# Kernel tuning notes

Hardware: AMD Instinct MI355X
Metric: run time of the kernel (lower is better)

The kernel has to match this reference:

```python
import jax, jax.numpy as jnp
import numpy as np

B, L1, L2 = 4, 1024, 512
D_PG, D_EX = 2304, 1024
H, HKV, DH = 8, 4, 256
SCALE = 256.0 ** -0.5


def _rope(x, cos, sin):
    # x: [B, L, h, DH]; cos/sin: [B, L, 1, DH//2]
    x = x.astype(jnp.float32)
    x1, x2 = jnp.split(x, 2, axis=-1)
    return jnp.concatenate([x1 * cos - x2 * sin, x2 * cos + x1 * sin], axis=-1)


def setup_inputs() -> dict:
    key = jax.random.key(0)
    ks = jax.random.split(key, 16)
    s = 0.02
    return {
        "pg_embeds": jax.random.normal(ks[0], (B, L1, D_PG), jnp.float32),
        "ex_embeds": jax.random.normal(ks[1], (B, L2, D_EX), jnp.float32),
        "cos": jax.random.normal(ks[2], (B, L1 + L2, 1, DH // 2), jnp.float32),
        "sin": jax.random.normal(ks[3], (B, L1 + L2, 1, DH // 2), jnp.float32),
        "attention_mask": jnp.zeros((B, L1 + L2, L1 + L2), jnp.float32),
        "Wq0": jax.random.normal(ks[4], (H * DH, D_PG), jnp.float32) * s,
        "Wk0": jax.random.normal(ks[5], (HKV * DH, D_PG), jnp.float32) * s,
        "Wv0": jax.random.normal(ks[6], (HKV * DH, D_PG), jnp.float32) * s,
        "Wo0": jax.random.normal(ks[7], (D_PG, H * DH), jnp.float32) * s,
        "Wq1": jax.random.normal(ks[8], (H * DH, D_EX), jnp.float32) * s,
        "Wk1": jax.random.normal(ks[9], (HKV * DH, D_EX), jnp.float32) * s,
        "Wv1": jax.random.normal(ks[10], (HKV * DH, D_EX), jnp.float32) * s,
        "Wo1": jax.random.normal(ks[11], (D_EX, H * DH), jnp.float32) * s,
    }


def reference(pg_embeds, ex_embeds, cos, sin, attention_mask,
              Wq0, Wk0, Wv0, Wo0, Wq1, Wk1, Wv1, Wo1):
    b, l1 = pg_embeds.shape[0], pg_embeds.shape[1]
    l2 = ex_embeds.shape[1]
    # per-stream QKV projections, then concat along sequence
    q = jnp.concatenate([
        (pg_embeds @ Wq0.T).reshape(b, l1, H, DH),
        (ex_embeds @ Wq1.T).reshape(b, l2, H, DH)], axis=1)
    k = jnp.concatenate([
        (pg_embeds @ Wk0.T).reshape(b, l1, HKV, DH),
        (ex_embeds @ Wk1.T).reshape(b, l2, HKV, DH)], axis=1)
    v = jnp.concatenate([
        (pg_embeds @ Wv0.T).reshape(b, l1, HKV, DH),
        (ex_embeds @ Wv1.T).reshape(b, l2, HKV, DH)], axis=1)
    q = _rope(q, cos, sin)  # fp32
    k = _rope(k, cos, sin)
    # GQA: repeat KV heads to match query heads
    rep = H // HKV
    k = jnp.repeat(k, rep, axis=2)
    v = jnp.repeat(jnp.repeat(v, rep, axis=2).astype(jnp.float32), 1, axis=0)
    # scores: [B, H, L, L]
    scores = jnp.einsum('bqhd,bkhd->bhqk', q, k) * SCALE
    scores = scores + attention_mask[:, None, :, :]
    p = jax.nn.softmax(scores, axis=-1)
    att = jnp.einsum('bhqk,bkhd->bqhd', p, v).reshape(b, l1 + l2, H * DH)
    out0 = att[:, :l1] @ Wo0.T
    out1 = att[:, l1:] @ Wo1.T
    return (out0, out1)
```

## Files before the change

kernel.cpp:

```cpp
#include <hip/hip_runtime.h>
#include <stdint.h>
#include <stddef.h>


typedef _Float16 f16;
typedef _Float16 f16x8 __attribute__((ext_vector_type(8)));
typedef _Float16 f16x4 __attribute__((ext_vector_type(4)));
typedef float    f32x4 __attribute__((ext_vector_type(4)));

__device__ __forceinline__ void async_ld16(const void* g, void* l) {
  __builtin_amdgcn_global_load_lds((const __attribute__((address_space(1))) void*)g,
                                   (__attribute__((address_space(3))) void*)l,
                                   16, 0, 0);
}

__device__ __forceinline__ int xswz(int bid, int n) {
  return (bid & 7) * (n >> 3) + (bid >> 3);
}

template <typename Epi>
__device__ __forceinline__ void gemm_pipe(f16* lds,
    const f16* __restrict__ A, int lda,
    const f16* __restrict__ B, int ldb,
    int K, Epi&& epi)
{
  const int t    = threadIdx.x;
  const int w    = t >> 6;
  const int lane = t & 63;
  const int q4   = lane >> 4;
  const int l16  = lane & 15;
  const int wm   = w >> 1;
  const int wn   = w & 1;

  const int srow = w * 16 + (lane >> 2);
  const int scol = (lane & 3) * 8;
  const f16* aP = A + (size_t)srow * lda + scol;
  const f16* bP = B + (size_t)srow * ldb + scol;
  const size_t a128 = (size_t)128 * lda;
  const int wl = w * 512;

  const int arow = (wm * 64 + l16) * 32 + q4 * 8;
  const int brow = (wn * 64 + l16) * 32 + q4 * 8;

  f32x4 acc[4][4];
  const f32x4 vz = {0.f, 0.f, 0.f, 0.f};
#pragma unroll
  for (int i = 0; i < 4; ++i)
#pragma unroll
    for (int j = 0; j < 4; ++j) acc[i][j] = vz;

#define STAGE3(kt, bi)                                            \
  { const int kk_ = (kt) << 5; f16* d_ = lds + (bi) * 12288;      \
    async_ld16(aP + kk_,        d_ + wl);                         \
    async_ld16(aP + a128 + kk_, d_ + 4096 + wl);                  \
    async_ld16(bP + kk_,        d_ + 8192 + wl); }

  STAGE3(0, 0);
  asm volatile("" ::: "memory");
  STAGE3(1, 1);

  const int NT = K >> 5;
  int cur = 0;
  for (int tk = 0; tk < NT; ++tk) {
    if (tk == NT - 1) asm volatile("s_waitcnt vmcnt(0)" ::: "memory");
    else              asm volatile("s_waitcnt vmcnt(3)" ::: "memory");
    asm volatile("s_barrier" ::: "memory");

    const f16* aS = lds + cur * 12288;
    const f16* bS = aS + 8192;
    f16x8 af[4], bf[4];
#pragma unroll
    for (int i = 0; i < 4; ++i) {
      af[i] = *(const f16x8*)(aS + arow + i * 512);
      bf[i] = *(const f16x8*)(bS + brow + i * 512);
    }
    if (tk + 2 < NT) {
      int nb = cur + 2; if (nb >= 3) nb -= 3;
      STAGE3(tk + 2, nb);
    }
    __builtin_amdgcn_s_setprio(1);
#pragma unroll
    for (int mi = 0; mi < 4; ++mi)
#pragma unroll
      for (int ni = 0; ni < 4; ++ni)
        acc[mi][ni] = __builtin_amdgcn_mfma_f32_16x16x32_f16(af[mi], bf[ni], acc[mi][ni], 0, 0, 0);
    __builtin_amdgcn_s_setprio(0);
    asm volatile("s_barrier" ::: "memory");
    ++cur; if (cur == 3) cur = 0;
  }
#undef STAGE3

#pragma unroll
  for (int mi = 0; mi < 4; ++mi)
#pragma unroll
    for (int ni = 0; ni < 4; ++ni)
#pragma unroll
      for (int r = 0; r < 4; ++r)
        epi(wm * 64 + mi * 16 + q4 * 4 + r, wn * 64 + ni * 16 + l16, acc[mi][ni][r]);
}

__global__ __launch_bounds__(512, 4) void k_qkv4(
    const f16* __restrict__ xpg, const f16* __restrict__ xex,
    const f16* __restrict__ W0,  const f16* __restrict__ W1,
    f16* __restrict__ q, f16* __restrict__ k, f16* __restrict__ v)
{
  __shared__ alignas(16) f16 lds[36864];
  const int idx = xswz(blockIdx.x, 768);
  int by, bx, K; const f16 *A, *B;
  const bool s0 = idx < 512;
  if (s0) { by = idx >> 5; bx = idx & 31; K = 2304;
            A = xpg + (size_t)by * 256 * 2304; B = W0 + (size_t)bx * 128 * 2304; }
  else    { int j = idx - 512; by = j >> 5; bx = j & 31; K = 1024;
            A = xex + (size_t)by * 256 * 1024; B = W1 + (size_t)bx * 128 * 1024; }

  f16* D; int ldd, coff;
  if (bx < 16)      { D = q; ldd = 2048; coff = 0; }
  else if (bx < 24) { D = k; ldd = 1024; coff = 2048; }
  else              { D = v; ldd = 1024; coff = 3072; }
  const int colb = bx * 128 - coff;
  const int rowb = s0 ? ((by >> 2) * 1536 + (by & 3) * 256)
                      : ((by >> 1) * 1536 + 1024 + (by & 1) * 256);

  gemm_pipe(lds, A, K, B, K, K, [&](int r, int c, float fv) {
    D[(size_t)(rowb + r) * ldd + colb + c] = (f16)fv;
  });
}

__global__ __launch_bounds__(256) void k_post(
    f16* __restrict__ q, f16* __restrict__ k,
    const float* __restrict__ cs, const float* __restrict__ sn,
    const float* __restrict__ msk, f16* __restrict__ mkh,
    const f16* __restrict__ v, f16* __restrict__ vt)
{
  const int blk = blockIdx.x;
  if (blk < 6144) {
    __shared__ f16 tile[32][33];
    const int b = blk / 1536, r0 = blk % 1536;
    const int d0 = (r0 & 31) * 32, l0 = (r0 >> 5) * 32;
    const int t = threadIdx.x;
    const int tr = t >> 5, tc = t & 31;
#pragma unroll
    for (int i = 0; i < 4; ++i)
      tile[tr + i * 8][tc] = v[((size_t)b * 1536 + l0 + tr + i * 8) * 1024 + d0 + tc];
    __syncthreads();
#pragma unroll
    for (int i = 0; i < 4; ++i) {
      int d = d0 + tr + i * 8;
      vt[(((size_t)b * 4 + (d >> 8)) * 256 + (d & 255)) * 1536 + l0 + tc] = tile[tc][tr + i * 8];
    }
  } else if (blk < 15360) {
    const size_t gid = ((size_t)(blk - 6144) * 256 + threadIdx.x) * 4;
    float4 m4 = *(const float4*)(msk + gid);
    f16x4 o = {(f16)m4.x, (f16)m4.y, (f16)m4.z, (f16)m4.w};
    *(f16x4*)(mkh + gid) = o;
  } else {
    const size_t tid8 = ((size_t)(blk - 15360) * 256 + threadIdx.x) * 8;
    f16* base; size_t row; int col;
    if (tid8 < 12582912ull) { base = q + tid8; row = tid8 >> 11; col = (int)(tid8 & 2047); }
    else { size_t f = tid8 - 12582912ull; base = k + f; row = f >> 10; col = (int)(f & 1023); }
    const int j0 = (col & 255) >> 1;
    f16x8 x = *(const f16x8*)base;
    float4 c4 = *(const float4*)(cs + row * 128 + j0);
    float4 s4 = *(const float4*)(sn + row * 128 + j0);
    f16x8 o;
    const float cc[4] = {c4.x, c4.y, c4.z, c4.w};
    const float ss[4] = {s4.x, s4.y, s4.z, s4.w};
#pragma unroll
    for (int p = 0; p < 4; ++p) {
      float x1 = (float)x[2 * p], x2 = (float)x[2 * p + 1];
      o[2 * p]     = (f16)(x1 * cc[p] - x2 * ss[p]);
      o[2 * p + 1] = (f16)(x2 * cc[p] + x1 * ss[p]);
    }
    *(f16x8*)base = o;
  }
}

__global__ __launch_bounds__(512, 4) void k_attn3(
    const f16* __restrict__ qb, const f16* __restrict__ kb,
    const f16* __restrict__ mask, f16* __restrict__ Sdst,
    const f16* __restrict__ Psrc, const f16* __restrict__ vt,
    f16* __restrict__ att0, f16* __restrict__ att1,
    const f16* __restrict__ wo0, const f16* __restrict__ wo1,
    float* __restrict__ out0, float* __restrict__ out1,
    int b_sc, int b_pv, int b_op, int npv, int nop)
{
  __shared__ alignas(16) f16 lds[36864];
  const int idx = xswz(blockIdx.x, (int)gridDim.x);
  if (idx < nop) {
    int by, bx, ldc, rowb; const f16 *A, *B; float* C;
    if (idx < 72) { by = idx / 18; bx = idx % 18;
                    A = att0 + (size_t)(b_op * 4 + by) * 256 * 2048;
                    B = wo0 + (size_t)bx * 128 * 2048;
                    C = out0; ldc = 2304; rowb = b_op * 1024 + by * 256; }
    else          { int j = idx - 72; by = j >> 3; bx = j & 7;
                    A = att1 + (size_t)(b_op * 2 + by) * 256 * 2048;
                    B = wo1 + (size_t)bx * 128 * 2048;
                    C = out1; ldc = 1024; rowb = b_op * 512 + by * 256; }
    const int colb = bx * 128;
    gemm_pipe(lds, A, 2048, B, 2048, 2048, [&](int r, int c, float fv) {
      C[(size_t)(rowb + r) * ldc + colb + c] = fv;
    });
  } else if (idx < nop + npv) {
    const int j = idx - nop;
    const int h = j / 12, rem = j % 12, by = rem >> 1, bx = rem & 1;
    const f16* A = Psrc + (size_t)h * 1536 * 1536 + (size_t)by * 256 * 1536;
    const f16* B = vt + (size_t)(b_pv * 4 + (h >> 1)) * 256 * 1536 + (size_t)bx * 128 * 1536;
    f16* dst = (by < 4)
      ? att0 + (size_t)(b_pv * 1024 + by * 256) * 2048 + h * 256 + bx * 128
      : att1 + (size_t)(b_pv * 512 + (by - 4) * 256) * 2048 + h * 256 + bx * 128;
    gemm_pipe(lds, A, 1536, B, 1536, 1536, [&](int r, int c, float fv) {
      dst[(size_t)r * 2048 + c] = (f16)fv;
    });
  } else {
    const int j = idx - nop - npv;
    const int h = j / 72, rem = j % 72, by = rem / 12, bx = rem % 12;
    const f16* A = qb + (size_t)b_sc * 1536 * 2048 + h * 256 + (size_t)by * 256 * 2048;
    const f16* B = kb + (size_t)b_sc * 1536 * 1024 + (h >> 1) * 256 + (size_t)bx * 128 * 1024;
    f16* Sz = Sdst + (size_t)h * 1536 * 1536 + (size_t)by * 256 * 1536 + bx * 128;
    const f16* mb = mask + (size_t)b_sc * 1536 * 1536 + (size_t)by * 256 * 1536 + bx * 128;
    gemm_pipe(lds, A, 2048, B, 1024, 256, [&](int r, int c, float fv) {
      size_t i = (size_t)r * 1536 + c;
      Sz[i] = (f16)(fv * 0.0625f + (float)mb[i]);
    });
  }
}

__global__ __launch_bounds__(256) void k_softmax(f16* __restrict__ S)
{
  const int row = blockIdx.x * 4 + (threadIdx.x >> 6);
  const int lane = threadIdx.x & 63;
  f16* p = S + (size_t)row * 1536 + lane * 8;
  f16x8 v0 = *(const f16x8*)p;
  f16x8 v1 = *(const f16x8*)(p + 512);
  f16x8 v2 = *(const f16x8*)(p + 1024);
  float x[24];
#pragma unroll
  for (int i = 0; i < 8; ++i) {
    x[i] = (float)v0[i]; x[8 + i] = (float)v1[i]; x[16 + i] = (float)v2[i];
  }
  float mx = x[0];
#pragma unroll
  for (int i = 1; i < 24; ++i) mx = fmaxf(mx, x[i]);
#pragma unroll
  for (int o = 32; o > 0; o >>= 1) mx = fmaxf(mx, __shfl_xor(mx, o, 64));
  float s = 0.f;
#pragma unroll
  for (int i = 0; i < 24; ++i) { x[i] = __expf(x[i] - mx); s += x[i]; }
#pragma unroll
  for (int o = 32; o > 0; o >>= 1) s += __shfl_xor(s, o, 64);
  const float inv = 1.f / s;
  f16x8 o0, o1, o2;
#pragma unroll
  for (int i = 0; i < 8; ++i) {
    o0[i] = (f16)(x[i] * inv); o1[i] = (f16)(x[8 + i] * inv); o2[i] = (f16)(x[16 + i] * inv);
  }
  *(f16x8*)p = o0; *(f16x8*)(p + 512) = o1; *(f16x8*)(p + 1024) = o2;
}

__global__ __launch_bounds__(256) void k_cast_all(
    const float* __restrict__ s0, const float* __restrict__ s1,
    const float* __restrict__ s2, const float* __restrict__ s3,
    const float* __restrict__ s4, const float* __restrict__ s5,
    f16* __restrict__ ws)
{
  const size_t gid = ((size_t)blockIdx.x * 256 + threadIdx.x) * 4;
  const float* s; size_t off, dst;
  if      (gid < 9437184ull)  { s = s0; off = gid;               dst = 0ull        + off; }
  else if (gid < 11534336ull) { s = s1; off = gid - 9437184ull;  dst = 9437184ull  + off; }
  else if (gid < 13893632ull) { s = s2; off = gid - 11534336ull; dst = 18612224ull + off; }
  else if (gid < 18612224ull) { s = s3; off = gid - 13893632ull; dst = 20971520ull + off; }
  else if (gid < 19660800ull) { s = s4; off = gid - 18612224ull; dst = 28835840ull + off; }
  else                        { s = s5; off = gid - 19660800ull; dst = 29884416ull + off; }
  float4 v = *(const float4*)(s + off);
  f16x4 o = {(f16)v.x, (f16)v.y, (f16)v.z, (f16)v.w};
  *(f16x4*)(ws + dst) = o;
}

__global__ __launch_bounds__(256) void k_cast_wr(
    const float* __restrict__ wq0, const float* __restrict__ wk0,
    const float* __restrict__ wq1, const float* __restrict__ wk1,
    f16* __restrict__ W0c, f16* __restrict__ W1c)
{
  const int idx = blockIdx.x;
  const float* src; f16* dstm; int K, r, drow;
  if      (idx < 2048) { src = wq0; dstm = W0c; K = 2304; r = idx;        drow = idx; }
  else if (idx < 3072) { src = wk0; dstm = W0c; K = 2304; r = idx - 2048; drow = idx; }
  else if (idx < 5120) { src = wq1; dstm = W1c; K = 1024; r = idx - 3072; drow = idx - 3072; }
  else                 { src = wk1; dstm = W1c; K = 1024; r = idx - 5120; drow = idx - 3072; }
  const int w = r & 255;
  const int srow = (r & ~255) + (w >> 1) + ((w & 1) << 7);
  const float* sp = src + (size_t)srow * K;
  f16* dp = dstm + (size_t)drow * K;
  for (int c = threadIdx.x * 4; c < K; c += 1024) {
    float4 v = *(const float4*)(sp + c);
    f16x4 o = {(f16)v.x, (f16)v.y, (f16)v.z, (f16)v.w};
    *(f16x4*)(dp + c) = o;
  }
}

extern "C" void kernel_launch(void* const* d_in, const int* in_sizes, int n_in,
                              void* d_out, int out_size, void* d_ws, size_t ws_size,
                              hipStream_t stream)
{
  (void)in_sizes; (void)n_in; (void)out_size; (void)ws_size;
  const float* pg  = (const float*)d_in[0];
  const float* ex  = (const float*)d_in[1];
  const float* cs  = (const float*)d_in[2];
  const float* sn  = (const float*)d_in[3];
  const float* msk = (const float*)d_in[4];

  char* ws = (char*)d_ws;
  f16* xpg  = (f16*)(ws + 0);
  f16* xex  = (f16*)(ws + 18874368);
  f16* W0c  = (f16*)(ws + 23068672);
  f16* wo0c = (f16*)(ws + 41943040);
  f16* W1c  = (f16*)(ws + 51380224);
  f16* wo1c = (f16*)(ws + 59768832);
  f16* qb   = (f16*)(ws + 63963136);
  f16* kb   = (f16*)(ws + 89128960);
  f16* vb   = (f16*)(ws + 101711872);
  f16* vt   = (f16*)(ws + 114294784);
  f16* att0 = (f16*)(ws + 126877696);
  f16* att1 = (f16*)(ws + 143654912);
  f16* S0   = (f16*)(ws + 152043520);
  f16* S1   = (f16*)(ws + 189792256);
  f16* mkh  = W0c;
  float* out0 = (float*)d_out;
  float* out1 = out0 + 9437184;

  k_cast_all<<<21248, 256, 0, stream>>>(
      pg, ex, (const float*)d_in[7], (const float*)d_in[8],
      (const float*)d_in[11], (const float*)d_in[12], (f16*)ws);
  k_cast_wr<<<6144, 256, 0, stream>>>(
      (const float*)d_in[5], (const float*)d_in[6],
      (const float*)d_in[9], (const float*)d_in[10], W0c, W1c);

  k_qkv4<<<768, 512, 0, stream>>>(xpg, xex, W0c, W1c, qb, kb, vb);

  k_post<<<24576, 256, 0, stream>>>(qb, kb, cs, sn, msk, mkh, vb, vt);

  k_attn3<<<576, 512, 0, stream>>>(qb, kb, mkh, S0, S0, vt, att0, att1, wo0c, wo1c, out0, out1, 0, 0, 0, 0, 0);
  k_softmax<<<3072, 256, 0, stream>>>(S0);
  k_attn3<<<672, 512, 0, stream>>>(qb, kb, mkh, S1, S0, vt, att0, att1, wo0c, wo1c, out0, out1, 1, 0, 0, 96, 0);
  k_softmax<<<3072, 256, 0, stream>>>(S1);
  k_attn3<<<760, 512, 0, stream>>>(qb, kb, mkh, S0, S1, vt, att0, att1, wo0c, wo1c, out0, out1, 2, 1, 0, 96, 88);
  k_softmax<<<3072, 256, 0, stream>>>(S0);
  k_attn3<<<760, 512, 0, stream>>>(qb, kb, mkh, S1, S0, vt, att0, att1, wo0c, wo1c, out0, out1, 3, 2, 1, 96, 88);
  k_softmax<<<3072, 256, 0, stream>>>(S1);

  k_attn3<<<184, 512, 0, stream>>>(qb, kb, mkh, S0, S1, vt, att0, att1, wo0c, wo1c, out0, out1, 0, 3, 2, 96, 88);
  k_attn3<<<88, 512, 0, stream>>>(qb, kb, mkh, S0, S1, vt, att0, att1, wo0c, wo1c, out0, out1, 0, 0, 3, 0, 88);
}
```

Measured before the change: 757.1 us.

## Enlarge GEMM tiles to 256x256 with double-buffered 64-wide K steps

Replaces the 256x128 triple-buffered GEMM core with a 256x256 tile that stages 64 K-elements per iteration into a double buffer, with each wave computing 128x64. Grid sizes for the QKV, QK^T, PV and output projection phases are halved, and the XCD block swizzle is dropped. The goal is more reuse per byte loaded into LDS and fewer blocks. In exchange it uses 128 KB LDS per block and twice the accumulators, which lowers occupancy to two blocks per CU. Small grids such as 44 or 92 blocks may also underfill the 256 CUs.

```diff
diff --git a/kernel.cpp b/kernel.cpp
--- a/kernel.cpp
+++ b/kernel.cpp
@@ -14,12 +14,8 @@
                                    16, 0, 0);
 }
 
-__device__ __forceinline__ int xswz(int bid, int n) {
-  return (bid & 7) * (n >> 3) + (bid >> 3);
-}
-
 template <typename Epi>
-__device__ __forceinline__ void gemm_pipe(f16* lds,
+__device__ __forceinline__ void gemm256(f16* lds,
     const f16* __restrict__ A, int lda,
     const f16* __restrict__ B, int ldb,
     int K, Epi&& epi)
@@ -29,99 +25,107 @@
   const int lane = t & 63;
   const int q4   = lane >> 4;
   const int l16  = lane & 15;
-  const int wm   = w >> 1;
-  const int wn   = w & 1;
-
-  const int srow = w * 16 + (lane >> 2);
-  const int scol = (lane & 3) * 8;
-  const f16* aP = A + (size_t)srow * lda + scol;
-  const f16* bP = B + (size_t)srow * ldb + scol;
-  const size_t a128 = (size_t)128 * lda;
-  const int wl = w * 512;
-
-  const int arow = (wm * 64 + l16) * 32 + q4 * 8;
+  const int wm   = w >> 2;
+  const int wn   = w & 3;
+
+  f16* ldsA = lds;
+  f16* ldsB = lds + 32768;
+
+  const f16* aP = A + (size_t)(lane >> 2) * lda + (lane & 3) * 8;
+  const f16* bP = B + (size_t)(lane >> 2) * ldb + (lane & 3) * 8;
+  const size_t aR0 = (size_t)(w * 32) * lda;
+  const size_t aR1 = aR0 + (size_t)16 * lda;
+  const size_t bR0 = (size_t)(w * 32) * ldb;
+  const size_t bR1 = bR0 + (size_t)16 * ldb;
+  const int wo = w * 1024;
+
+  const int arow = (wm * 128 + l16) * 32 + q4 * 8;
   const int brow = (wn * 64 + l16) * 32 + q4 * 8;
 
-  f32x4 acc[4][4];
+  f32x4 acc[8][4];
   const f32x4 vz = {0.f, 0.f, 0.f, 0.f};
 #pragma unroll
-  for (int i = 0; i < 4; ++i)
+  for (int i = 0; i < 8; ++i)
 #pragma unroll
     for (int j = 0; j < 4; ++j) acc[i][j] = vz;
 
-#define STAGE3(kt, bi)                                            \
-  { const int kk_ = (kt) << 5; f16* d_ = lds + (bi) * 12288;      \
-    async_ld16(aP + kk_,        d_ + wl);                         \
-    async_ld16(aP + a128 + kk_, d_ + 4096 + wl);                  \
-    async_ld16(bP + kk_,        d_ + 8192 + wl); }
-
-  STAGE3(0, 0);
-  asm volatile("" ::: "memory");
-  STAGE3(1, 1);
-
-  const int NT = K >> 5;
-  int cur = 0;
+#pragma unroll
+  for (int s = 0; s < 2; ++s) {
+    const int kk = s * 32;
+    async_ld16(aP + aR0 + kk, ldsA + s * 8192 + wo);
+    async_ld16(aP + aR1 + kk, ldsA + s * 8192 + wo + 512);
+    async_ld16(bP + bR0 + kk, ldsB + s * 8192 + wo);
+    async_ld16(bP + bR1 + kk, ldsB + s * 8192 + wo + 512);
+  }
+
+  const int NT = K >> 6;
   for (int tk = 0; tk < NT; ++tk) {
-    if (tk == NT - 1) asm volatile("s_waitcnt vmcnt(0)" ::: "memory");
-    else              asm volatile("s_waitcnt vmcnt(3)" ::: "memory");
-    asm volatile("s_barrier" ::: "memory");
-
-    const f16* aS = lds + cur * 12288;
-    const f16* bS = aS + 8192;
-    f16x8 af[4], bf[4];
-#pragma unroll
-    for (int i = 0; i < 4; ++i) {
-      af[i] = *(const f16x8*)(aS + arow + i * 512);
-      bf[i] = *(const f16x8*)(bS + brow + i * 512);
+    const int d  = (tk & 1) ? 16384 : 0;
+    const int dn = 16384 - d;
+    const bool st = tk + 1 < NT;
+    const int kn = (tk + 1) << 6;
+#pragma unroll
+    for (int s = 0; s < 2; ++s) {
+      if (s == 0 || st) asm volatile("s_waitcnt vmcnt(4)" ::: "memory");
+      else              asm volatile("s_waitcnt vmcnt(0)" ::: "memory");
+      asm volatile("s_barrier" ::: "memory");
+      const f16* aS = ldsA + d + s * 8192;
+      const f16* bS = ldsB + d + s * 8192;
+      f16x8 af[8], bf[4];
+#pragma unroll
+      for (int i = 0; i < 8; ++i) af[i] = *(const f16x8*)(aS + arow + i * 512);
+#pragma unroll
+      for (int i = 0; i < 4; ++i) bf[i] = *(const f16x8*)(bS + brow + i * 512);
+      if (st) {
+        const int kk = kn + s * 32;
+        async_ld16(aP + aR0 + kk, ldsA + dn + s * 8192 + wo);
+        async_ld16(aP + aR1 + kk, ldsA + dn + s * 8192 + wo + 512);
+        async_ld16(bP + bR0 + kk, ldsB + dn + s * 8192 + wo);
+        async_ld16(bP + bR1 + kk, ldsB + dn + s * 8192 + wo + 512);
+      }
+      __builtin_amdgcn_s_setprio(1);
+#pragma unroll
+      for (int mi = 0; mi < 8; ++mi)
+#pragma unroll
+        for (int ni = 0; ni < 4; ++ni)
+          acc[mi][ni] = __builtin_amdgcn_mfma_f32_16x16x32_f16(af[mi], bf[ni], acc[mi][ni], 0, 0, 0);
+      __builtin_amdgcn_s_setprio(0);
+      asm volatile("s_barrier" ::: "memory");
     }
-    if (tk + 2 < NT) {
-      int nb = cur + 2; if (nb >= 3) nb -= 3;
-      STAGE3(tk + 2, nb);
-    }
-    __builtin_amdgcn_s_setprio(1);
-#pragma unroll
-    for (int mi = 0; mi < 4; ++mi)
-#pragma unroll
-      for (int ni = 0; ni < 4; ++ni)
-        acc[mi][ni] = __builtin_amdgcn_mfma_f32_16x16x32_f16(af[mi], bf[ni], acc[mi][ni], 0, 0, 0);
-    __builtin_amdgcn_s_setprio(0);
-    asm volatile("s_barrier" ::: "memory");
-    ++cur; if (cur == 3) cur = 0;
-  }
-#undef STAGE3
-
-#pragma unroll
-  for (int mi = 0; mi < 4; ++mi)
+  }
+
+#pragma unroll
+  for (int mi = 0; mi < 8; ++mi)
 #pragma unroll
     for (int ni = 0; ni < 4; ++ni)
 #pragma unroll
       for (int r = 0; r < 4; ++r)
-        epi(wm * 64 + mi * 16 + q4 * 4 + r, wn * 64 + ni * 16 + l16, acc[mi][ni][r]);
-}
-
-__global__ __launch_bounds__(512, 4) void k_qkv4(
+        epi(wm * 128 + mi * 16 + q4 * 4 + r, wn * 64 + ni * 16 + l16, acc[mi][ni][r]);
+}
+
+__global__ __launch_bounds__(512, 2) void k_qkv5(
     const f16* __restrict__ xpg, const f16* __restrict__ xex,
     const f16* __restrict__ W0,  const f16* __restrict__ W1,
     f16* __restrict__ q, f16* __restrict__ k, f16* __restrict__ v)
 {
-  __shared__ alignas(16) f16 lds[36864];
-  const int idx = xswz(blockIdx.x, 768);
+  __shared__ alignas(16) f16 lds[65536];
+  const int idx = blockIdx.x;
   int by, bx, K; const f16 *A, *B;
-  const bool s0 = idx < 512;
-  if (s0) { by = idx >> 5; bx = idx & 31; K = 2304;
-            A = xpg + (size_t)by * 256 * 2304; B = W0 + (size_t)bx * 128 * 2304; }
-  else    { int j = idx - 512; by = j >> 5; bx = j & 31; K = 1024;
-            A = xex + (size_t)by * 256 * 1024; B = W1 + (size_t)bx * 128 * 1024; }
+  const bool s0 = idx < 256;
+  if (s0) { by = idx >> 4; bx = idx & 15; K = 2304;
+            A = xpg + (size_t)by * 256 * 2304; B = W0 + (size_t)bx * 256 * 2304; }
+  else    { int j = idx - 256; by = j >> 4; bx = j & 15; K = 1024;
+            A = xex + (size_t)by * 256 * 1024; B = W1 + (size_t)bx * 256 * 1024; }
 
   f16* D; int ldd, coff;
-  if (bx < 16)      { D = q; ldd = 2048; coff = 0; }
-  else if (bx < 24) { D = k; ldd = 1024; coff = 2048; }
+  if (bx < 8)       { D = q; ldd = 2048; coff = 0; }
+  else if (bx < 12) { D = k; ldd = 1024; coff = 2048; }
   else              { D = v; ldd = 1024; coff = 3072; }
-  const int colb = bx * 128 - coff;
+  const int colb = bx * 256 - coff;
   const int rowb = s0 ? ((by >> 2) * 1536 + (by & 3) * 256)
                       : ((by >> 1) * 1536 + 1024 + (by & 1) * 256);
 
-  gemm_pipe(lds, A, K, B, K, K, [&](int r, int c, float fv) {
+  gemm256(lds, A, K, B, K, K, [&](int r, int c, float fv) {
     D[(size_t)(rowb + r) * ldd + colb + c] = (f16)fv;
   });
 }
@@ -175,7 +179,7 @@
   }
 }
 
-__global__ __launch_bounds__(512, 4) void k_attn3(
+__global__ __launch_bounds__(512, 2) void k_attn4(
     const f16* __restrict__ qb, const f16* __restrict__ kb,
     const f16* __restrict__ mask, f16* __restrict__ Sdst,
     const f16* __restrict__ Psrc, const f16* __restrict__ vt,
@@ -184,41 +188,41 @@
     float* __restrict__ out0, float* __restrict__ out1,
     int b_sc, int b_pv, int b_op, int npv, int nop)
 {
-  __shared__ alignas(16) f16 lds[36864];
-  const int idx = xswz(blockIdx.x, (int)gridDim.x);
+  __shared__ alignas(16) f16 lds[65536];
+  const int idx = blockIdx.x;
   if (idx < nop) {
     int by, bx, ldc, rowb; const f16 *A, *B; float* C;
-    if (idx < 72) { by = idx / 18; bx = idx % 18;
+    if (idx < 36) { by = idx / 9; bx = idx % 9;
                     A = att0 + (size_t)(b_op * 4 + by) * 256 * 2048;
-                    B = wo0 + (size_t)bx * 128 * 2048;
+                    B = wo0 + (size_t)bx * 256 * 2048;
                     C = out0; ldc = 2304; rowb = b_op * 1024 + by * 256; }
-    else          { int j = idx - 72; by = j >> 3; bx = j & 7;
+    else          { int j = idx - 36; by = j >> 2; bx = j & 3;
                     A = att1 + (size_t)(b_op * 2 + by) * 256 * 2048;
-                    B = wo1 + (size_t)bx * 128 * 2048;
+                    B = wo1 + (size_t)bx * 256 * 2048;
                     C = out1; ldc = 1024; rowb = b_op * 512 + by * 256; }
-    const int colb = bx * 128;
-    gemm_pipe(lds, A, 2048, B, 2048, 2048, [&](int r, int c, float fv) {
+    const int colb = bx * 256;
+    gemm256(lds, A, 2048, B, 2048, 2048, [&](int r, int c, float fv) {
       C[(size_t)(rowb + r) * ldc + colb + c] = fv;
     });
   } else if (idx < nop + npv) {
     const int j = idx - nop;
-    const int h = j / 12, rem = j % 12, by = rem >> 1, bx = rem & 1;
+    const int h = j / 6, by = j % 6;
     const f16* A = Psrc + (size_t)h * 1536 * 1536 + (size_t)by * 256 * 1536;
-    const f16* B = vt + (size_t)(b_pv * 4 + (h >> 1)) * 256 * 1536 + (size_t)bx * 128 * 1536;
+    const f16* B = vt + (size_t)(b_pv * 4 + (h >> 1)) * 256 * 1536;
     f16* dst = (by < 4)
-      ? att0 + (size_t)(b_pv * 1024 + by * 256) * 2048 + h * 256 + bx * 128
-      : att1 + (size_t)(b_pv * 512 + (by - 4) * 256) * 2048 + h * 256 + bx * 128;
-    gemm_pipe(lds, A, 1536, B, 1536, 1536, [&](int r, int c, float fv) {
+      ? att0 + (size_t)(b_pv * 1024 + by * 256) * 2048 + h * 256
+      : att1 + (size_t)(b_pv * 512 + (by - 4) * 256) * 2048 + h * 256;
+    gemm256(lds, A, 1536, B, 1536, 1536, [&](int r, int c, float fv) {
       dst[(size_t)r * 2048 + c] = (f16)fv;
     });
   } else {
     const int j = idx - nop - npv;
-    const int h = j / 72, rem = j % 72, by = rem / 12, bx = rem % 12;
+    const int h = j / 36, rem = j % 36, by = rem / 6, bx = rem % 6;
     const f16* A = qb + (size_t)b_sc * 1536 * 2048 + h * 256 + (size_t)by * 256 * 2048;
-    const f16* B = kb + (size_t)b_sc * 1536 * 1024 + (h >> 1) * 256 + (size_t)bx * 128 * 1024;
-    f16* Sz = Sdst + (size_t)h * 1536 * 1536 + (size_t)by * 256 * 1536 + bx * 128;
-    const f16* mb = mask + (size_t)b_sc * 1536 * 1536 + (size_t)by * 256 * 1536 + bx * 128;
-    gemm_pipe(lds, A, 2048, B, 1024, 256, [&](int r, int c, float fv) {
+    const f16* B = kb + (size_t)b_sc * 1536 * 1024 + (h >> 1) * 256 + (size_t)bx * 256 * 1024;
+    f16* Sz = Sdst + (size_t)h * 1536 * 1536 + (size_t)by * 256 * 1536 + bx * 256;
+    const f16* mb = mask + (size_t)b_sc * 1536 * 1536 + (size_t)by * 256 * 1536 + bx * 256;
+    gemm256(lds, A, 2048, B, 1024, 256, [&](int r, int c, float fv) {
       size_t i = (size_t)r * 1536 + c;
       Sz[i] = (f16)(fv * 0.0625f + (float)mb[i]);
     });
@@ -335,19 +339,19 @@
       (const float*)d_in[5], (const float*)d_in[6],
       (const float*)d_in[9], (const float*)d_in[10], W0c, W1c);
 
-  k_qkv4<<<768, 512, 0, stream>>>(xpg, xex, W0c, W1c, qb, kb, vb);
+  k_qkv5<<<384, 512, 0, stream>>>(xpg, xex, W0c, W1c, qb, kb, vb);
 
   k_post<<<24576, 256, 0, stream>>>(qb, kb, cs, sn, msk, mkh, vb, vt);
 
-  k_attn3<<<576, 512, 0, stream>>>(qb, kb, mkh, S0, S0, vt, att0, att1, wo0c, wo1c, out0, out1, 0, 0, 0, 0, 0);
+  k_attn4<<<288, 512, 0, stream>>>(qb, kb, mkh, S0, S0, vt, att0, att1, wo0c, wo1c, out0, out1, 0, 0, 0, 0, 0);
   k_softmax<<<3072, 256, 0, stream>>>(S0);
-  k_attn3<<<672, 512, 0, stream>>>(qb, kb, mkh, S1, S0, vt, att0, att1, wo0c, wo1c, out0, out1, 1, 0, 0, 96, 0);
+  k_attn4<<<336, 512, 0, stream>>>(qb, kb, mkh, S1, S0, vt, att0, att1, wo0c, wo1c, out0, out1, 1, 0, 0, 48, 0);
   k_softmax<<<3072, 256, 0, stream>>>(S1);
-  k_attn3<<<760, 512, 0, stream>>>(qb, kb, mkh, S0, S1, vt, att0, att1, wo0c, wo1c, out0, out1, 2, 1, 0, 96, 88);
+  k_attn4<<<380, 512, 0, stream>>>(qb, kb, mkh, S0, S1, vt, att0, att1, wo0c, wo1c, out0, out1, 2, 1, 0, 48, 44);
   k_softmax<<<3072, 256, 0, stream>>>(S0);
-  k_attn3<<<760, 512, 0, stream>>>(qb, kb, mkh, S1, S0, vt, att0, att1, wo0c, wo1c, out0, out1, 3, 2, 1, 96, 88);
+  k_attn4<<<380, 512, 0, stream>>>(qb, kb, mkh, S1, S0, vt, att0, att1, wo0c, wo1c, out0, out1, 3, 2, 1, 48, 44);
   k_softmax<<<3072, 256, 0, stream>>>(S1);
 
-  k_attn3<<<184, 512, 0, stream>>>(qb, kb, mkh, S0, S1, vt, att0, att1, wo0c, wo1c, out0, out1, 0, 3, 2, 96, 88);
-  k_attn3<<<88, 512, 0, stream>>>(qb, kb, mkh, S0, S1, vt, att0, att1, wo0c, wo1c, out0, out1, 0, 0, 3, 0, 88);
-}
+  k_attn4<<<92, 512, 0, stream>>>(qb, kb, mkh, S0, S1, vt, att0, att1, wo0c, wo1c, out0, out1, 0, 3, 2, 48, 44);
+  k_attn4<<<44, 512, 0, stream>>>(qb, kb, mkh, S0, S1, vt, att0, att1, wo0c, wo1c, out0, out1, 0, 0, 3, 0, 44);
+}
```

Result: faster. 682.2 us (-9.9%).
